# Performance work log

Hardware: AMD Instinct MI355X
Metric: run time of the kernel (lower is better)

Reference implementation:

```python
import jax, jax.numpy as jnp
import numpy as np

B, CIN, COUT, H, W, K, G = 2, 256, 256, 128, 128, 3, 4
PAD = (K - 1) // 2


def setup_inputs() -> dict:
    key = jax.random.key(0)
    k1, k2, k3, k4 = jax.random.split(key, 4)
    x = jax.random.normal(k1, (B, CIN, H, W), dtype=jnp.float32)
    # conv_offset: 1x1 conv, out channels = G*2*K*K. (Zero-init in the module; use
    # small random weights so offsets are non-trivial for correctness testing.)
    w_offset = jax.random.normal(k2, (G * 2 * K * K, CIN), dtype=jnp.float32) * 0.01
    b_offset = jax.random.normal(k3, (G * 2 * K * K,), dtype=jnp.float32) * 0.5
    # DeformConv weight (bias=False in mmcv DeformConv)
    w_deform = jax.random.normal(k4, (COUT, CIN, K, K), dtype=jnp.float32) * (1.0 / np.sqrt(CIN * K * K))
    return {"x": x, "w_offset": w_offset, "b_offset": b_offset, "w_deform": w_deform}


def _bilinear_gather(img, y, x):
    """img: [B,G,Cg,H,W]; y,x: [B,G,H,W] float sample coords -> [B,G,Cg,H,W].
    Zero padding outside the image (mmcv DCN bilinear semantics)."""
    b, g, cg, h, w = img.shape
    imgf = img.reshape(b, g, cg, h * w)
    y0 = jnp.floor(y)
    x0 = jnp.floor(x)
    out = jnp.zeros((b, g, cg, h * w), img.dtype)
    for yy, xx in ((y0, x0), (y0, x0 + 1.0), (y0 + 1.0, x0), (y0 + 1.0, x0 + 1.0)):
        wgt = (1.0 - jnp.abs(y - yy)) * (1.0 - jnp.abs(x - xx))
        valid = (yy >= 0) & (yy < h) & (xx >= 0) & (xx < w)
        wgt = jnp.where(valid, wgt, 0.0)
        yi = jnp.clip(yy, 0, h - 1).astype(jnp.int32)
        xi = jnp.clip(xx, 0, w - 1).astype(jnp.int32)
        idx = (yi * w + xi).reshape(b, g, 1, h * w)
        vals = jnp.take_along_axis(imgf, jnp.broadcast_to(idx, (b, g, cg, h * w)), axis=3)
        out = out + wgt.reshape(b, g, 1, h * w) * vals
    return out.reshape(b, g, cg, h, w)


def reference(x, w_offset, b_offset, w_deform):
    b, cin, h, w = x.shape
    cout, _, k, _ = w_deform.shape
    pad = (k - 1) // 2
    # 1x1 offset conv
    offset = jnp.einsum('bchw,oc->bohw', x, w_offset) + b_offset[None, :, None, None]
    g = offset.shape[1] // (2 * k * k)
    off = offset.reshape(b, g, k * k, 2, h, w)  # (dy, dx) per kernel tap, mmcv layout
    xg = x.reshape(b, g, cin // g, h, w)
    hh = jnp.arange(h, dtype=x.dtype)[:, None]
    ww = jnp.arange(w, dtype=x.dtype)[None, :]
    out = jnp.zeros((b, cout, h, w), x.dtype)
    for i in range(k):
        for j in range(k):
            t = i * k + j
            ys = hh - pad + i + off[:, :, t, 0]  # [B,G,H,W]
            xs = ww - pad + j + off[:, :, t, 1]
            samp = _bilinear_gather(xg, ys, xs).reshape(b, cin, h, w)
            out = out + jnp.einsum('bchw,oc->bohw', samp, w_deform[:, :, i, j])
    return jax.nn.relu(out)
```

## Files before the change

### kernel.cpp

```cpp
#include <hip/hip_runtime.h>
#include <stdint.h>

#define HW    16384
#define CIN   256
#define COUT  256
#define Hh    128
#define Ww    128
#define OFFC  72

typedef __attribute__((ext_vector_type(4))) float    f32x4;
typedef __attribute__((ext_vector_type(2))) _Float16 f16x2;
typedef __attribute__((ext_vector_type(8))) _Float16 f16x8;
typedef unsigned short u16;
typedef unsigned int   u32;

__device__ __forceinline__ u16 f2h(float f) { return __builtin_bit_cast(u16, (_Float16)f); }
__device__ __forceinline__ u32 pk2(float f) { u32 h = f2h(f); return h | (h << 16); }
__device__ __forceinline__ f16x2 bch(u32 u) { return __builtin_bit_cast(f16x2, u); }

__device__ __forceinline__ void bar_nodrain() {
  asm volatile("s_waitcnt lgkmcnt(0)" ::: "memory");
  __builtin_amdgcn_sched_barrier(0);
  __builtin_amdgcn_s_barrier();
  __builtin_amdgcn_sched_barrier(0);
}

__global__ __launch_bounds__(256) void kprep(const float* __restrict__ x, const float* __restrict__ wd,
                                             const float* __restrict__ wo, u16* __restrict__ xt,
                                             u16* __restrict__ wfrag, u16* __restrict__ wfrag2) {
  __shared__ float smem[64 * 129];
  int blk = blockIdx.x;
  if (blk < 1024) {
    int bg = blk >> 7;
    int p0 = (blk & 127) << 7;
    const float* src = x + (size_t)bg * 64 * HW + p0;
    #pragma unroll
    for (int r = 0; r < 8; ++r) {
      int idx = (threadIdx.x + 256 * r) * 4;
      int c = idx >> 7, px = idx & 127;
      f32x4 v = *(const f32x4*)(src + (size_t)c * HW + px);
      smem[c * 129 + px + 0] = v[0];
      smem[c * 129 + px + 1] = v[1];
      smem[c * 129 + px + 2] = v[2];
      smem[c * 129 + px + 3] = v[3];
    }
    __syncthreads();
    u16* dstb = xt + ((size_t)bg * HW + p0) * 64;
    #pragma unroll
    for (int k = 0; k < 4; ++k) {
      int e  = k * 256 + threadIdx.x;
      int px = e >> 3, ck = e & 7;
      u32 w[4];
      #pragma unroll
      for (int m = 0; m < 4; ++m) {
        float lo = smem[(ck * 8 + 2 * m + 0) * 129 + px];
        float hi = smem[(ck * 8 + 2 * m + 1) * 129 + px];
        w[m] = (u32)f2h(lo) | ((u32)f2h(hi) << 16);
      }
      *(uint4*)(dstb + (size_t)e * 8) = make_uint4(w[0], w[1], w[2], w[3]);
    }
  } else if (blk < 1152) {
    int bb = blk - 1024;
    int nh = bb & 31;
    int g  = bb >> 5;
    const float* src = wd + (size_t)(nh * 8) * 2304 + (size_t)g * 64 * 9;
    #pragma unroll
    for (int r = 0; r < 18; ++r) {
      int idx = threadIdx.x + 256 * r;
      int cl  = idx / 576;
      int rem = idx - cl * 576;
      smem[cl * 576 + rem] = src[(size_t)cl * 2304 + rem];
    }
    __syncthreads();
    int nt = nh >> 1, nb = (nh & 1) * 8;
    #pragma unroll
    for (int r = 0; r < 18; ++r) {
      int o  = threadIdx.x + 256 * r;
      int j  = o & 7;
      int n8 = (o >> 3) & 7;
      int q  = (o >> 6) & 3;
      int kcl = o >> 8;
      int t = kcl >> 1, half = kcl & 1;
      int cg = half * 32 + q * 8 + j;
      float v = smem[n8 * 576 + cg * 9 + t];
      int kc = (g * 9 + t) * 2 + half;
      int lane = q * 16 + nb + n8;
      wfrag[((size_t)(kc * 16 + nt) * 64 + lane) * 8 + j] = f2h(v);
    }
  } else {
    int e = (blk - 1152) * 256 + threadIdx.x;
    int j = e & 7;
    int lane = (e >> 3) & 63;
    int idx = e >> 9;
    int kc = idx / 5, nt = idx - 5 * kc;
    int n16 = lane & 15, q = lane >> 4;
    int oc = nt * 16 + n16;
    int c  = kc * 32 + q * 8 + j;
    float v = (oc < OFFC) ? wo[(size_t)oc * CIN + c] : 0.f;
    wfrag2[e] = f2h(v);
  }
}

__device__ __forceinline__ void mkpre(float yy, float xx, int* ob, u32* wp) {
  float y0f = floorf(yy), x0f = floorf(xx);
  float fy = yy - y0f, fx = xx - x0f;
  int y0 = (int)y0f, x0 = (int)x0f;
  int y1 = y0 + 1, x1 = x0 + 1;
  float vy0 = (y0 >= 0 && y0 < Hh) ? 1.f : 0.f;
  float vy1 = (y1 >= 0 && y1 < Hh) ? 1.f : 0.f;
  float vx0 = (x0 >= 0 && x0 < Ww) ? 1.f : 0.f;
  float vx1 = (x1 >= 0 && x1 < Ww) ? 1.f : 0.f;
  wp[0] = pk2((1.f - fy) * (1.f - fx) * vy0 * vx0);
  wp[1] = pk2((1.f - fy) * fx * vy0 * vx1);
  wp[2] = pk2(fy * (1.f - fx) * vy1 * vx0);
  wp[3] = pk2(fy * fx * vy1 * vx1);
  int cy0 = min(max(y0, 0), Hh - 1), cy1 = min(max(y1, 0), Hh - 1);
  int cx0 = min(max(x0, 0), Ww - 1), cx1 = min(max(x1, 0), Ww - 1);
  ob[0] = (cy0 * Ww + cx0) << 7;
  ob[1] = (cy0 * Ww + cx1) << 7;
  ob[2] = (cy1 * Ww + cx0) << 7;
  ob[3] = (cy1 * Ww + cx1) << 7;
}

__device__ __forceinline__ uint4 bil16(const uint4* v, const u32* wp) {
  f16x2 W0 = bch(wp[0]), W1 = bch(wp[1]), W2 = bch(wp[2]), W3 = bch(wp[3]);
  uint4 r;
  { f16x2 s = bch(v[0].x) * W0 + bch(v[1].x) * W1 + bch(v[2].x) * W2 + bch(v[3].x) * W3; r.x = __builtin_bit_cast(u32, s); }
  { f16x2 s = bch(v[0].y) * W0 + bch(v[1].y) * W1 + bch(v[2].y) * W2 + bch(v[3].y) * W3; r.y = __builtin_bit_cast(u32, s); }
  { f16x2 s = bch(v[0].z) * W0 + bch(v[1].z) * W1 + bch(v[2].z) * W2 + bch(v[3].z) * W3; r.z = __builtin_bit_cast(u32, s); }
  { f16x2 s = bch(v[0].w) * W0 + bch(v[1].w) * W1 + bch(v[2].w) * W2 + bch(v[3].w) * W3; r.w = __builtin_bit_cast(u32, s); }
  return r;
}

__global__ __launch_bounds__(512) void k2(const u16* __restrict__ xt, const u16* __restrict__ wfrag2,
                                          const float* __restrict__ bo, const u16* __restrict__ wfrag,
                                          float* __restrict__ out) {
  __shared__ u16   astage[2 * 8 * 512];
  __shared__ float offl[64 * 74];
  int tid  = threadIdx.x;
  int lane = tid & 63, n16 = lane & 15, q = (tid >> 4) & 3;
  int wv   = tid >> 6;
  int sp   = wv >> 1;
  int hp   = wv & 1;
  int b  = blockIdx.x >> 8;
  int p0 = (blockIdx.x & 255) << 6;
  int h  = p0 >> 7, w0 = p0 & 127;
  const char* xtb = (const char*)xt + (size_t)b * 4 * HW * 128;
  float fh  = (float)h;
  float fxp = (float)(w0 + sp * 16 + n16);
  int   chb = hp * 64 + q * 16;

  f32x4 acc[4][2];
  #pragma unroll
  for (int mt = 0; mt < 4; ++mt) {
    acc[mt][0] = (f32x4){0.f, 0.f, 0.f, 0.f};
    acc[mt][1] = (f32x4){0.f, 0.f, 0.f, 0.f};
  }

  if (wv < 4) {
    f32x4 oacc[5];
    #pragma unroll
    for (int nt = 0; nt < 5; ++nt) {
      int oc = nt * 16 + n16;
      float bv = (oc < OFFC) ? bo[oc] : 0.f;
      oacc[nt] = (f32x4){bv, bv, bv, bv};
    }
    #pragma unroll
    for (int kc = 0; kc < 8; ++kc) {
      int g = kc >> 1;
      f16x8 af = __builtin_bit_cast(f16x8, *(const uint4*)(xtb +
          ((size_t)(g * HW + p0 + wv * 16 + n16)) * 128 + (kc & 1) * 64 + q * 16));
      #pragma unroll
      for (int nt = 0; nt < 5; ++nt) {
        f16x8 bfo = __builtin_bit_cast(f16x8, *(const uint4*)(wfrag2 + (size_t)(((kc * 5 + nt) << 6) + lane) * 8));
        oacc[nt] = __builtin_amdgcn_mfma_f32_16x16x32_f16(af, bfo, oacc[nt], 0, 0, 0);
      }
    }
    #pragma unroll
    for (int nt = 0; nt < 5; ++nt) {
      int oc = nt * 16 + n16;
      if (oc < OFFC) {
        #pragma unroll
        for (int r = 0; r < 4; ++r)
          offl[(wv * 16 + q * 4 + r) * 74 + oc] = oacc[nt][r];
      }
    }
  }
  uint4 bf0[2];
  bf0[0] = *(const uint4*)(wfrag + ((size_t)(wv * 2 + 0) * 64 + lane) * 8);
  bf0[1] = *(const uint4*)(wfrag + ((size_t)(wv * 2 + 1) * 64 + lane) * 8);
  __syncthreads();

  uint4 dA[4], dB[4];
  u32   wpA[4], wpB[4];

  auto issue = [&](int gt, uint4* dd, u32* wpp) {
    int pxl = sp * 16 + n16;
    float oy = offl[pxl * 74 + gt * 2];
    float ox = offl[pxl * 74 + gt * 2 + 1];
    int g = (gt * 57) >> 9;
    int t = gt - g * 9;
    int i = (t * 683) >> 11;
    int j = t - i * 3;
    int ob[4];
    mkpre(fh + (float)(i - 1) + oy, fxp + (float)(j - 1) + ox, ob, wpp);
    const char* xg = xtb + (size_t)g * HW * 128;
    #pragma unroll
    for (int c = 0; c < 4; ++c)
      dd[c] = *(const uint4*)(xg + ob[c] + chb);
  };
  auto consume = [&](int slot, int gt) {
    uint4 bf1[2];
    const u16* wb1 = wfrag + ((size_t)((2 * gt + 1) * 16 + wv * 2) * 64 + lane) * 8;
    bf1[0] = *(const uint4*)(wb1);
    bf1[1] = *(const uint4*)(wb1 + 512);
    __builtin_amdgcn_s_setprio(1);
    #pragma unroll
    for (int mt = 0; mt < 4; ++mt) {
      f16x8 af = __builtin_bit_cast(f16x8,
          *(const uint4*)&astage[(slot * 8 + mt * 2 + 0) * 512 + lane * 8]);
      acc[mt][0] = __builtin_amdgcn_mfma_f32_16x16x32_f16(af, __builtin_bit_cast(f16x8, bf0[0]), acc[mt][0], 0, 0, 0);
      acc[mt][1] = __builtin_amdgcn_mfma_f32_16x16x32_f16(af, __builtin_bit_cast(f16x8, bf0[1]), acc[mt][1], 0, 0, 0);
    }
    #pragma unroll
    for (int mt = 0; mt < 4; ++mt) {
      f16x8 af = __builtin_bit_cast(f16x8,
          *(const uint4*)&astage[(slot * 8 + mt * 2 + 1) * 512 + lane * 8]);
      acc[mt][0] = __builtin_amdgcn_mfma_f32_16x16x32_f16(af, __builtin_bit_cast(f16x8, bf1[0]), acc[mt][0], 0, 0, 0);
      acc[mt][1] = __builtin_amdgcn_mfma_f32_16x16x32_f16(af, __builtin_bit_cast(f16x8, bf1[1]), acc[mt][1], 0, 0, 0);
    }
    __builtin_amdgcn_s_setprio(0);
    if (gt < 35) {
      const u16* wb0 = wfrag + ((size_t)((2 * gt + 2) * 16 + wv * 2) * 64 + lane) * 8;
      bf0[0] = *(const uint4*)(wb0);
      bf0[1] = *(const uint4*)(wb0 + 512);
    }
  };

  issue(0, dA, wpA);
  issue(1, dB, wpB);
  *(uint4*)&astage[(0 * 8 + sp * 2 + hp) * 512 + lane * 8] = bil16(dA, wpA);
  bar_nodrain();

  #pragma unroll 1
  for (int gt = 0; gt < 36; gt += 2) {
    *(uint4*)&astage[(1 * 8 + sp * 2 + hp) * 512 + lane * 8] = bil16(dB, wpB);
    if (gt + 2 < 36) issue(gt + 2, dA, wpA);
    consume(0, gt);
    bar_nodrain();
    if (gt + 2 < 36) {
      *(uint4*)&astage[(0 * 8 + sp * 2 + hp) * 512 + lane * 8] = bil16(dA, wpA);
      issue(gt + 3, dB, wpB);
    }
    consume(1, gt + 1);
    bar_nodrain();
  }

  float* op = out + (size_t)b * COUT * HW + p0;
  #pragma unroll
  for (int mt = 0; mt < 4; ++mt)
    #pragma unroll
    for (int j = 0; j < 2; ++j) {
      f32x4 v = acc[mt][j];
      #pragma unroll
      for (int r = 0; r < 4; ++r) v[r] = fmaxf(v[r], 0.f);
      int cout = wv * 32 + j * 16 + n16;
      *(f32x4*)(op + (size_t)cout * HW + mt * 16 + q * 4) = v;
    }
}

extern "C" void kernel_launch(void* const* d_in, const int* in_sizes, int n_in,
                              void* d_out, int out_size, void* d_ws, size_t ws_size,
                              hipStream_t stream) {
  const float* x  = (const float*)d_in[0];
  const float* wo = (const float*)d_in[1];
  const float* bo = (const float*)d_in[2];
  const float* wd = (const float*)d_in[3];
  float* out = (float*)d_out;

  u16* xtp    = (u16*)d_ws;
  u16* wfrag  = (u16*)((char*)d_ws + 16777216);
  u16* wfrag2 = (u16*)((char*)d_ws + 16777216 + 1179648);

  kprep<<<1232, 256, 0, stream>>>(x, wd, wo, xtp, wfrag, wfrag2);
  k2   <<<512,  512, 0, stream>>>(xtp, wfrag2, bo, wfrag, out);
}
```

Baseline: 198.2 us.

## Drop LDS staging; each wave gathers its own A tile and splits Cout

The k2 kernel no longer shares bilinear-sampled A fragments through LDS with barriers. Each wave now samples all 64 channels of a group tap for its 16 pixels directly in registers and computes half of the output channels (128), so waves partition work over pixels and Cout halves. This removes per-tap LDS writes, reads and block barriers. The cost is that each bilinear gather is duplicated across the two Cout-half waves, and B weight fragments are loaded from global memory every tap with no prefetch. Launch bounds add a minimum-occupancy hint of 4.

```diff
diff --git a/kernel.cpp b/kernel.cpp
--- a/kernel.cpp
+++ b/kernel.cpp
@@ -17,13 +17,6 @@
 __device__ __forceinline__ u16 f2h(float f) { return __builtin_bit_cast(u16, (_Float16)f); }
 __device__ __forceinline__ u32 pk2(float f) { u32 h = f2h(f); return h | (h << 16); }
 __device__ __forceinline__ f16x2 bch(u32 u) { return __builtin_bit_cast(f16x2, u); }
-
-__device__ __forceinline__ void bar_nodrain() {
-  asm volatile("s_waitcnt lgkmcnt(0)" ::: "memory");
-  __builtin_amdgcn_sched_barrier(0);
-  __builtin_amdgcn_s_barrier();
-  __builtin_amdgcn_sched_barrier(0);
-}
 
 __global__ __launch_bounds__(256) void kprep(const float* __restrict__ x, const float* __restrict__ wd,
                                              const float* __restrict__ wo, u16* __restrict__ xt,
@@ -122,40 +115,36 @@
   ob[3] = (cy1 * Ww + cx1) << 7;
 }
 
-__device__ __forceinline__ uint4 bil16(const uint4* v, const u32* wp) {
+__device__ __forceinline__ f16x8 bil16(const uint4* v, const u32* wp) {
   f16x2 W0 = bch(wp[0]), W1 = bch(wp[1]), W2 = bch(wp[2]), W3 = bch(wp[3]);
   uint4 r;
   { f16x2 s = bch(v[0].x) * W0 + bch(v[1].x) * W1 + bch(v[2].x) * W2 + bch(v[3].x) * W3; r.x = __builtin_bit_cast(u32, s); }
   { f16x2 s = bch(v[0].y) * W0 + bch(v[1].y) * W1 + bch(v[2].y) * W2 + bch(v[3].y) * W3; r.y = __builtin_bit_cast(u32, s); }
   { f16x2 s = bch(v[0].z) * W0 + bch(v[1].z) * W1 + bch(v[2].z) * W2 + bch(v[3].z) * W3; r.z = __builtin_bit_cast(u32, s); }
   { f16x2 s = bch(v[0].w) * W0 + bch(v[1].w) * W1 + bch(v[2].w) * W2 + bch(v[3].w) * W3; r.w = __builtin_bit_cast(u32, s); }
-  return r;
-}
-
-__global__ __launch_bounds__(512) void k2(const u16* __restrict__ xt, const u16* __restrict__ wfrag2,
-                                          const float* __restrict__ bo, const u16* __restrict__ wfrag,
-                                          float* __restrict__ out) {
-  __shared__ u16   astage[2 * 8 * 512];
+  return __builtin_bit_cast(f16x8, r);
+}
+
+__global__ __launch_bounds__(512, 4) void k2(const u16* __restrict__ xt, const u16* __restrict__ wfrag2,
+                                             const float* __restrict__ bo, const u16* __restrict__ wfrag,
+                                             float* __restrict__ out) {
   __shared__ float offl[64 * 74];
   int tid  = threadIdx.x;
   int lane = tid & 63, n16 = lane & 15, q = (tid >> 4) & 3;
   int wv   = tid >> 6;
-  int sp   = wv >> 1;
-  int hp   = wv & 1;
+  int sp   = wv & 3;
+  int ch   = wv >> 2;
   int b  = blockIdx.x >> 8;
   int p0 = (blockIdx.x & 255) << 6;
   int h  = p0 >> 7, w0 = p0 & 127;
   const char* xtb = (const char*)xt + (size_t)b * 4 * HW * 128;
   float fh  = (float)h;
   float fxp = (float)(w0 + sp * 16 + n16);
-  int   chb = hp * 64 + q * 16;
-
-  f32x4 acc[4][2];
+  int   q16 = q * 16;
+
+  f32x4 acc[8];
   #pragma unroll
-  for (int mt = 0; mt < 4; ++mt) {
-    acc[mt][0] = (f32x4){0.f, 0.f, 0.f, 0.f};
-    acc[mt][1] = (f32x4){0.f, 0.f, 0.f, 0.f};
-  }
+  for (int nt = 0; nt < 8; ++nt) acc[nt] = (f32x4){0.f, 0.f, 0.f, 0.f};
 
   if (wv < 4) {
     f32x4 oacc[5];
@@ -186,87 +175,65 @@
       }
     }
   }
-  uint4 bf0[2];
-  bf0[0] = *(const uint4*)(wfrag + ((size_t)(wv * 2 + 0) * 64 + lane) * 8);
-  bf0[1] = *(const uint4*)(wfrag + ((size_t)(wv * 2 + 1) * 64 + lane) * 8);
   __syncthreads();
 
-  uint4 dA[4], dB[4];
+  int   pxl = sp * 16 + n16;
+  int   ob[4];
   u32   wpA[4], wpB[4];
-
-  auto issue = [&](int gt, uint4* dd, u32* wpp) {
-    int pxl = sp * 16 + n16;
+  uint4 d0[4], d1[4];
+
+  auto prep = [&](int gt, u32* wp) {
     float oy = offl[pxl * 74 + gt * 2];
     float ox = offl[pxl * 74 + gt * 2 + 1];
     int g = (gt * 57) >> 9;
     int t = gt - g * 9;
     int i = (t * 683) >> 11;
     int j = t - i * 3;
-    int ob[4];
-    mkpre(fh + (float)(i - 1) + oy, fxp + (float)(j - 1) + ox, ob, wpp);
-    const char* xg = xtb + (size_t)g * HW * 128;
-    #pragma unroll
-    for (int c = 0; c < 4; ++c)
-      dd[c] = *(const uint4*)(xg + ob[c] + chb);
+    mkpre(fh + (float)(i - 1) + oy, fxp + (float)(j - 1) + ox, ob, wp);
+    int gb = g * (HW * 128) + q16;
+    #pragma unroll
+    for (int c = 0; c < 4; ++c) ob[c] += gb;
   };
-  auto consume = [&](int slot, int gt) {
-    uint4 bf1[2];
-    const u16* wb1 = wfrag + ((size_t)((2 * gt + 1) * 16 + wv * 2) * 64 + lane) * 8;
-    bf1[0] = *(const uint4*)(wb1);
-    bf1[1] = *(const uint4*)(wb1 + 512);
-    __builtin_amdgcn_s_setprio(1);
-    #pragma unroll
-    for (int mt = 0; mt < 4; ++mt) {
-      f16x8 af = __builtin_bit_cast(f16x8,
-          *(const uint4*)&astage[(slot * 8 + mt * 2 + 0) * 512 + lane * 8]);
-      acc[mt][0] = __builtin_amdgcn_mfma_f32_16x16x32_f16(af, __builtin_bit_cast(f16x8, bf0[0]), acc[mt][0], 0, 0, 0);
-      acc[mt][1] = __builtin_amdgcn_mfma_f32_16x16x32_f16(af, __builtin_bit_cast(f16x8, bf0[1]), acc[mt][1], 0, 0, 0);
-    }
-    #pragma unroll
-    for (int mt = 0; mt < 4; ++mt) {
-      f16x8 af = __builtin_bit_cast(f16x8,
-          *(const uint4*)&astage[(slot * 8 + mt * 2 + 1) * 512 + lane * 8]);
-      acc[mt][0] = __builtin_amdgcn_mfma_f32_16x16x32_f16(af, __builtin_bit_cast(f16x8, bf1[0]), acc[mt][0], 0, 0, 0);
-      acc[mt][1] = __builtin_amdgcn_mfma_f32_16x16x32_f16(af, __builtin_bit_cast(f16x8, bf1[1]), acc[mt][1], 0, 0, 0);
-    }
-    __builtin_amdgcn_s_setprio(0);
-    if (gt < 35) {
-      const u16* wb0 = wfrag + ((size_t)((2 * gt + 2) * 16 + wv * 2) * 64 + lane) * 8;
-      bf0[0] = *(const uint4*)(wb0);
-      bf0[1] = *(const uint4*)(wb0 + 512);
+  auto gload = [&]() {
+    #pragma unroll
+    for (int c = 0; c < 4; ++c) {
+      d0[c] = *(const uint4*)(xtb + ob[c]);
+      d1[c] = *(const uint4*)(xtb + ob[c] + 64);
     }
   };
-
-  issue(0, dA, wpA);
-  issue(1, dB, wpB);
-  *(uint4*)&astage[(0 * 8 + sp * 2 + hp) * 512 + lane * 8] = bil16(dA, wpA);
-  bar_nodrain();
-
+  auto mm = [&](int gt, f16x8 a0, f16x8 a1) {
+    const u16* wb = wfrag + ((size_t)((gt * 2) * 16 + ch * 8) * 64 + lane) * 8;
+    #pragma unroll
+    for (int nt = 0; nt < 8; ++nt) {
+      f16x8 b0 = __builtin_bit_cast(f16x8, *(const uint4*)(wb + nt * 512));
+      f16x8 b1 = __builtin_bit_cast(f16x8, *(const uint4*)(wb + 8192 + nt * 512));
+      acc[nt] = __builtin_amdgcn_mfma_f32_16x16x32_f16(a0, b0, acc[nt], 0, 0, 0);
+      acc[nt] = __builtin_amdgcn_mfma_f32_16x16x32_f16(a1, b1, acc[nt], 0, 0, 0);
+    }
+  };
+
+  prep(0, wpA); gload();
   #pragma unroll 1
   for (int gt = 0; gt < 36; gt += 2) {
-    *(uint4*)&astage[(1 * 8 + sp * 2 + hp) * 512 + lane * 8] = bil16(dB, wpB);
-    if (gt + 2 < 36) issue(gt + 2, dA, wpA);
-    consume(0, gt);
-    bar_nodrain();
-    if (gt + 2 < 36) {
-      *(uint4*)&astage[(0 * 8 + sp * 2 + hp) * 512 + lane * 8] = bil16(dA, wpA);
-      issue(gt + 3, dB, wpB);
-    }
-    consume(1, gt + 1);
-    bar_nodrain();
-  }
-
-  float* op = out + (size_t)b * COUT * HW + p0;
+    f16x8 a0 = bil16(d0, wpA);
+    f16x8 a1 = bil16(d1, wpA);
+    prep(gt + 1, wpB); gload();
+    mm(gt, a0, a1);
+    a0 = bil16(d0, wpB);
+    a1 = bil16(d1, wpB);
+    if (gt + 2 < 36) { prep(gt + 2, wpA); gload(); }
+    mm(gt + 1, a0, a1);
+  }
+
+  float* op = out + (size_t)b * COUT * HW + p0 + sp * 16;
   #pragma unroll
-  for (int mt = 0; mt < 4; ++mt)
-    #pragma unroll
-    for (int j = 0; j < 2; ++j) {
-      f32x4 v = acc[mt][j];
-      #pragma unroll
-      for (int r = 0; r < 4; ++r) v[r] = fmaxf(v[r], 0.f);
-      int cout = wv * 32 + j * 16 + n16;
-      *(f32x4*)(op + (size_t)cout * HW + mt * 16 + q * 4) = v;
-    }
+  for (int nt = 0; nt < 8; ++nt) {
+    f32x4 v = acc[nt];
+    #pragma unroll
+    for (int r = 0; r < 4; ++r) v[r] = fmaxf(v[r], 0.f);
+    int cout = ch * 128 + nt * 16 + n16;
+    *(f32x4*)(op + (size_t)cout * HW + q * 4) = v;
+  }
 }
 
 extern "C" void kernel_launch(void* const* d_in, const int* in_sizes, int n_in,
```

Result: slower. 279.5 us (+41.0%).

## Shrink k2 tiles to 32 pixels with 4 waves and swizzle block order

Applied to the files above, without the earlier changes.

The main kernel now processes 32 pixels per block with 4 waves instead of 64 pixels with 8 waves. Each wave covers 64 output channels over 2 M-tiles, so it loads 4 weight fragments per step instead of 2. The grid doubles to 1024 blocks, with a blockIdx swizzle so co-resident blocks touch spatially spread regions, and launch bounds request 4 blocks per CU. The gather pipeline is simplified to a single register buffer, and the scheduling barriers and setprio hints are removed. The intent is better occupancy and load balance, at the cost of twice the weight-fragment traffic per output pixel and more register pressure.

```diff
diff --git a/kernel.cpp b/kernel.cpp
--- a/kernel.cpp
+++ b/kernel.cpp
@@ -18,11 +18,10 @@
 __device__ __forceinline__ u32 pk2(float f) { u32 h = f2h(f); return h | (h << 16); }
 __device__ __forceinline__ f16x2 bch(u32 u) { return __builtin_bit_cast(f16x2, u); }
 
-__device__ __forceinline__ void bar_nodrain() {
+__device__ __forceinline__ void bar() {
   asm volatile("s_waitcnt lgkmcnt(0)" ::: "memory");
-  __builtin_amdgcn_sched_barrier(0);
   __builtin_amdgcn_s_barrier();
-  __builtin_amdgcn_sched_barrier(0);
+  asm volatile("" ::: "memory");
 }
 
 __global__ __launch_bounds__(256) void kprep(const float* __restrict__ x, const float* __restrict__ wd,
@@ -132,32 +131,34 @@
   return r;
 }
 
-__global__ __launch_bounds__(512) void k2(const u16* __restrict__ xt, const u16* __restrict__ wfrag2,
-                                          const float* __restrict__ bo, const u16* __restrict__ wfrag,
-                                          float* __restrict__ out) {
-  __shared__ u16   astage[2 * 8 * 512];
-  __shared__ float offl[64 * 74];
+__global__ __launch_bounds__(256, 4) void k2(const u16* __restrict__ xt, const u16* __restrict__ wfrag2,
+                                             const float* __restrict__ bo, const u16* __restrict__ wfrag,
+                                             float* __restrict__ out) {
+  __shared__ u16   astage[2 * 4 * 512];
+  __shared__ float offl[32 * 74];
   int tid  = threadIdx.x;
   int lane = tid & 63, n16 = lane & 15, q = (tid >> 4) & 3;
   int wv   = tid >> 6;
-  int sp   = wv >> 1;
-  int hp   = wv & 1;
-  int b  = blockIdx.x >> 8;
-  int p0 = (blockIdx.x & 255) << 6;
+  int sp   = wv & 1;
+  int hp   = wv >> 1;
+  int blk  = blockIdx.x;
+  int swz  = (blk & 7) * 128 + (blk >> 3);
+  int b  = swz >> 9;
+  int p0 = (swz & 511) << 5;
   int h  = p0 >> 7, w0 = p0 & 127;
   const char* xtb = (const char*)xt + (size_t)b * 4 * HW * 128;
   float fh  = (float)h;
   float fxp = (float)(w0 + sp * 16 + n16);
   int   chb = hp * 64 + q * 16;
-
-  f32x4 acc[4][2];
+  int   pxl = sp * 16 + n16;
+
+  f32x4 acc[2][4];
   #pragma unroll
-  for (int mt = 0; mt < 4; ++mt) {
-    acc[mt][0] = (f32x4){0.f, 0.f, 0.f, 0.f};
-    acc[mt][1] = (f32x4){0.f, 0.f, 0.f, 0.f};
-  }
-
-  if (wv < 4) {
+  for (int mt = 0; mt < 2; ++mt)
+    #pragma unroll
+    for (int i = 0; i < 4; ++i) acc[mt][i] = (f32x4){0.f, 0.f, 0.f, 0.f};
+
+  if (wv < 2) {
     f32x4 oacc[5];
     #pragma unroll
     for (int nt = 0; nt < 5; ++nt) {
@@ -186,16 +187,16 @@
       }
     }
   }
-  uint4 bf0[2];
-  bf0[0] = *(const uint4*)(wfrag + ((size_t)(wv * 2 + 0) * 64 + lane) * 8);
-  bf0[1] = *(const uint4*)(wfrag + ((size_t)(wv * 2 + 1) * 64 + lane) * 8);
+  uint4 bf0[4];
+  #pragma unroll
+  for (int i = 0; i < 4; ++i)
+    bf0[i] = *(const uint4*)(wfrag + ((size_t)(4 * wv + i) * 64 + lane) * 8);
   __syncthreads();
 
-  uint4 dA[4], dB[4];
-  u32   wpA[4], wpB[4];
-
-  auto issue = [&](int gt, uint4* dd, u32* wpp) {
-    int pxl = sp * 16 + n16;
+  uint4 d[4];
+  u32   wp[4];
+
+  auto pg = [&](int gt) {
     float oy = offl[pxl * 74 + gt * 2];
     float ox = offl[pxl * 74 + gt * 2 + 1];
     int g = (gt * 57) >> 9;
@@ -203,68 +204,68 @@
     int i = (t * 683) >> 11;
     int j = t - i * 3;
     int ob[4];
-    mkpre(fh + (float)(i - 1) + oy, fxp + (float)(j - 1) + ox, ob, wpp);
+    mkpre(fh + (float)(i - 1) + oy, fxp + (float)(j - 1) + ox, ob, wp);
     const char* xg = xtb + (size_t)g * HW * 128;
     #pragma unroll
     for (int c = 0; c < 4; ++c)
-      dd[c] = *(const uint4*)(xg + ob[c] + chb);
+      d[c] = *(const uint4*)(xg + ob[c] + chb);
   };
   auto consume = [&](int slot, int gt) {
-    uint4 bf1[2];
-    const u16* wb1 = wfrag + ((size_t)((2 * gt + 1) * 16 + wv * 2) * 64 + lane) * 8;
-    bf1[0] = *(const uint4*)(wb1);
-    bf1[1] = *(const uint4*)(wb1 + 512);
-    __builtin_amdgcn_s_setprio(1);
-    #pragma unroll
-    for (int mt = 0; mt < 4; ++mt) {
+    uint4 bf1[4];
+    const u16* wb1 = wfrag + ((size_t)((2 * gt + 1) * 16 + 4 * wv) * 64 + lane) * 8;
+    #pragma unroll
+    for (int i = 0; i < 4; ++i) bf1[i] = *(const uint4*)(wb1 + i * 512);
+    #pragma unroll
+    for (int mt = 0; mt < 2; ++mt) {
       f16x8 af = __builtin_bit_cast(f16x8,
-          *(const uint4*)&astage[(slot * 8 + mt * 2 + 0) * 512 + lane * 8]);
-      acc[mt][0] = __builtin_amdgcn_mfma_f32_16x16x32_f16(af, __builtin_bit_cast(f16x8, bf0[0]), acc[mt][0], 0, 0, 0);
-      acc[mt][1] = __builtin_amdgcn_mfma_f32_16x16x32_f16(af, __builtin_bit_cast(f16x8, bf0[1]), acc[mt][1], 0, 0, 0);
-    }
-    #pragma unroll
-    for (int mt = 0; mt < 4; ++mt) {
+          *(const uint4*)&astage[(slot * 4 + mt * 2 + 0) * 512 + lane * 8]);
+      #pragma unroll
+      for (int i = 0; i < 4; ++i)
+        acc[mt][i] = __builtin_amdgcn_mfma_f32_16x16x32_f16(af, __builtin_bit_cast(f16x8, bf0[i]), acc[mt][i], 0, 0, 0);
+    }
+    #pragma unroll
+    for (int mt = 0; mt < 2; ++mt) {
       f16x8 af = __builtin_bit_cast(f16x8,
-          *(const uint4*)&astage[(slot * 8 + mt * 2 + 1) * 512 + lane * 8]);
-      acc[mt][0] = __builtin_amdgcn_mfma_f32_16x16x32_f16(af, __builtin_bit_cast(f16x8, bf1[0]), acc[mt][0], 0, 0, 0);
-      acc[mt][1] = __builtin_amdgcn_mfma_f32_16x16x32_f16(af, __builtin_bit_cast(f16x8, bf1[1]), acc[mt][1], 0, 0, 0);
-    }
-    __builtin_amdgcn_s_setprio(0);
+          *(const uint4*)&astage[(slot * 4 + mt * 2 + 1) * 512 + lane * 8]);
+      #pragma unroll
+      for (int i = 0; i < 4; ++i)
+        acc[mt][i] = __builtin_amdgcn_mfma_f32_16x16x32_f16(af, __builtin_bit_cast(f16x8, bf1[i]), acc[mt][i], 0, 0, 0);
+    }
     if (gt < 35) {
-      const u16* wb0 = wfrag + ((size_t)((2 * gt + 2) * 16 + wv * 2) * 64 + lane) * 8;
-      bf0[0] = *(const uint4*)(wb0);
-      bf0[1] = *(const uint4*)(wb0 + 512);
+      const u16* wb0 = wfrag + ((size_t)((2 * gt + 2) * 16 + 4 * wv) * 64 + lane) * 8;
+      #pragma unroll
+      for (int i = 0; i < 4; ++i) bf0[i] = *(const uint4*)(wb0 + i * 512);
     }
   };
 
-  issue(0, dA, wpA);
-  issue(1, dB, wpB);
-  *(uint4*)&astage[(0 * 8 + sp * 2 + hp) * 512 + lane * 8] = bil16(dA, wpA);
-  bar_nodrain();
+  pg(0);
+  *(uint4*)&astage[(0 * 4 + sp * 2 + hp) * 512 + lane * 8] = bil16(d, wp);
+  pg(1);
+  bar();
 
   #pragma unroll 1
-  for (int gt = 0; gt < 36; gt += 2) {
-    *(uint4*)&astage[(1 * 8 + sp * 2 + hp) * 512 + lane * 8] = bil16(dB, wpB);
-    if (gt + 2 < 36) issue(gt + 2, dA, wpA);
-    consume(0, gt);
-    bar_nodrain();
-    if (gt + 2 < 36) {
-      *(uint4*)&astage[(0 * 8 + sp * 2 + hp) * 512 + lane * 8] = bil16(dA, wpA);
-      issue(gt + 3, dB, wpB);
-    }
-    consume(1, gt + 1);
-    bar_nodrain();
+  for (int t = 0; t < 36; t += 2) {
+    *(uint4*)&astage[(1 * 4 + sp * 2 + hp) * 512 + lane * 8] = bil16(d, wp);
+    if (t + 2 < 36) pg(t + 2);
+    consume(0, t);
+    bar();
+    if (t + 2 < 36) {
+      *(uint4*)&astage[(0 * 4 + sp * 2 + hp) * 512 + lane * 8] = bil16(d, wp);
+      if (t + 3 < 36) pg(t + 3);
+    }
+    consume(1, t + 1);
+    bar();
   }
 
   float* op = out + (size_t)b * COUT * HW + p0;
   #pragma unroll
-  for (int mt = 0; mt < 4; ++mt)
-    #pragma unroll
-    for (int j = 0; j < 2; ++j) {
-      f32x4 v = acc[mt][j];
+  for (int mt = 0; mt < 2; ++mt)
+    #pragma unroll
+    for (int i = 0; i < 4; ++i) {
+      f32x4 v = acc[mt][i];
       #pragma unroll
       for (int r = 0; r < 4; ++r) v[r] = fmaxf(v[r], 0.f);
-      int cout = wv * 32 + j * 16 + n16;
+      int cout = wv * 64 + i * 16 + n16;
       *(f32x4*)(op + (size_t)cout * HW + mt * 16 + q * 4) = v;
     }
 }
@@ -283,5 +284,5 @@
   u16* wfrag2 = (u16*)((char*)d_ws + 16777216 + 1179648);
 
   kprep<<<1232, 256, 0, stream>>>(x, wd, wo, xtp, wfrag, wfrag2);
-  k2   <<<512,  512, 0, stream>>>(xtp, wfrag2, bo, wfrag, out);
-}
+  k2   <<<1024, 256, 0, stream>>>(xtp, wfrag2, bo, wfrag, out);
+}
```

Measured after the change: 192.4 us. 1.03x faster.
